# Performance work log

Measured on AMD Instinct MI355X. Metric: run time of the kernel, lower is better.

Reference implementation:

```python
import jax, jax.numpy as jnp
import numpy as np
import math

DMODEL, DK, H, DFF = 1024, 64, 16, 4096
B, T = 2, 2048
EPS = 1e-5


def setup_inputs() -> dict:
    key = jax.random.key(0)
    ks = jax.random.split(key, 12)
    s = 0.02
    x = jax.random.normal(ks[0], (B, T, DMODEL), dtype=jnp.float32)
    # causal mask, broadcastable [1,1,T,T]; 0 -> masked (like masked_fill(mask==0, -inf))
    attention_mask = jnp.tril(jnp.ones((T, T), dtype=jnp.int32))[None, None]
    Wq = jax.random.normal(ks[1], (DMODEL, DK * H), dtype=jnp.float32) * s
    bq = jnp.zeros((DK * H,), jnp.float32)
    Wk = jax.random.normal(ks[2], (DMODEL, DK * H), dtype=jnp.float32) * s
    bk = jnp.zeros((DK * H,), jnp.float32)
    Wv = jax.random.normal(ks[3], (DMODEL, DMODEL), dtype=jnp.float32) * s
    bv = jnp.zeros((DMODEL,), jnp.float32)
    W1 = jax.random.normal(ks[4], (DMODEL, DFF), dtype=jnp.float32) * s
    b1 = jnp.zeros((DFF,), jnp.float32)
    W2 = jax.random.normal(ks[5], (DFF, DMODEL), dtype=jnp.float32) * s
    b2 = jnp.zeros((DMODEL,), jnp.float32)
    g1 = jnp.ones((DMODEL,), jnp.float32)
    be1 = jnp.zeros((DMODEL,), jnp.float32)
    g2 = jnp.ones((DMODEL,), jnp.float32)
    be2 = jnp.zeros((DMODEL,), jnp.float32)
    return dict(x=x, attention_mask=attention_mask, Wq=Wq, bq=bq, Wk=Wk, bk=bk,
                Wv=Wv, bv=bv, W1=W1, b1=b1, W2=W2, b2=b2,
                g1=g1, be1=be1, g2=g2, be2=be2)


def _layernorm(x, g, b):
    mu = jnp.mean(x, axis=-1, keepdims=True)
    var = jnp.mean(jnp.square(x - mu), axis=-1, keepdims=True)
    return (x - mu) * jax.lax.rsqrt(var + EPS) * g + b


def _split_heads(t, h):  # [B,T,h*d] -> [B,h,T,d]
    Bn, Tn, D = t.shape
    return t.reshape(Bn, Tn, h, D // h).transpose(0, 2, 1, 3)


def reference(x, attention_mask, Wq, bq, Wk, bk, Wv, bv, W1, b1, W2, b2, g1, be1, g2, be2):
    # multi-head self-attention (hand-rolled, matching torch module)
    q = _split_heads(x @ Wq + bq, H)                    # [B,h,T,dk]
    k = _split_heads(x @ Wk + bk, H)                    # [B,h,T,dk]
    v = _split_heads(x @ Wv + bv, H)                    # [B,h,T,dv]
    scores = jnp.einsum('bhqd,bhkd->bhqk', q, k) / math.sqrt(DK)
    scores = jnp.where(attention_mask == 0, -jnp.inf, scores)
    probs = jax.nn.softmax(scores, axis=-1)
    attn = jnp.einsum('bhqk,bhkd->bhqd', probs, v)      # [B,h,T,dv]
    attn = attn.transpose(0, 2, 1, 3).reshape(B, T, DMODEL)
    # double residual (dropout = identity in eval): x + dropout(attn) + attn
    x1 = _layernorm(x + 2.0 * attn, g1, be1)
    ff = jax.nn.relu(x1 @ W1 + b1) @ W2 + b2
    out = _layernorm(x1 + 2.0 * ff, g2, be2)
    return out
```

## Files before the change

### kernel.cpp

```cpp
#include <hip/hip_runtime.h>

#define DMODEL 1024
#define DKH 64
#define NH 16
#define DFF 4096
#define BB 2
#define TT 2048
#define ROWS (BB*TT)
#define QKVN (3*DMODEL)

typedef unsigned short ushort_t;
typedef __attribute__((ext_vector_type(8))) short s8v;
typedef __attribute__((ext_vector_type(4))) float f4v;
typedef __attribute__((ext_vector_type(4))) unsigned short us4v;

typedef const void __attribute__((address_space(1)))* GPTR;
typedef void __attribute__((address_space(3)))* SPTR;

__device__ __forceinline__ float bf2f(ushort_t u) {
  return __uint_as_float(((unsigned int)u) << 16);
}
__device__ __forceinline__ ushort_t f2bf(float f) {
  unsigned int u = __float_as_uint(f);
  u += 0x7fffu + ((u >> 16) & 1u);
  return (ushort_t)(u >> 16);
}
__device__ __forceinline__ void gload16(const void* g, void* l) {
  __builtin_amdgcn_global_load_lds((GPTR)g, (SPTR)l, 16, 0, 0);
}

__global__ __launch_bounds__(256) void cvt_f32_bf16(const float* __restrict__ in,
                                                    ushort_t* __restrict__ out, int n4) {
  int i = blockIdx.x * 256 + threadIdx.x;
  if (i >= n4) return;
  float4 v = ((const float4*)in)[i];
  us4v o;
  o.x = f2bf(v.x); o.y = f2bf(v.y); o.z = f2bf(v.z); o.w = f2bf(v.w);
  ((us4v*)out)[i] = o;
}

__global__ __launch_bounds__(256) void transpose_cvt(const float* __restrict__ in,
                                                     ushort_t* __restrict__ out, int R, int C) {
  __shared__ float tile[32][33];
  int bx = blockIdx.x * 32, by = blockIdx.y * 32;
  int tx = threadIdx.x, ty = threadIdx.y;
#pragma unroll
  for (int i = 0; i < 32; i += 8)
    tile[ty + i][tx] = in[(size_t)(by + ty + i) * C + bx + tx];
  __syncthreads();
#pragma unroll
  for (int i = 0; i < 32; i += 8)
    out[(size_t)(bx + ty + i) * R + by + tx] = f2bf(tile[tx][ty + i]);
}

__global__ void concat_bias(const float* __restrict__ a, const float* __restrict__ b,
                            const float* __restrict__ c, float* __restrict__ o) {
  int i = blockIdx.x * 256 + threadIdx.x;
  if (i < 1024) { o[i] = a[i]; o[1024 + i] = b[i]; o[2048 + i] = c[i]; }
}

__global__ __launch_bounds__(256) void vtrans(const ushort_t* __restrict__ QKV,
                                              ushort_t* __restrict__ VT) {
  __shared__ ushort_t tile[32][66];
  const int t0 = blockIdx.x * 32;
  const int bh = blockIdx.y;
  const int b = bh >> 4, h = bh & 15;
  const int tx = threadIdx.x, ty = threadIdx.y;
  const ushort_t* src = QKV + ((size_t)b * TT + t0) * QKVN + 2 * DMODEL + h * 64;
#pragma unroll
  for (int i = 0; i < 4; ++i) {
    int r = ty + i * 8;
    *(unsigned int*)&tile[r][tx * 2] = *(const unsigned int*)(src + (size_t)r * QKVN + tx * 2);
  }
  __syncthreads();
  unsigned int* dst = (unsigned int*)(VT + (size_t)bh * 64 * TT);
#pragma unroll
  for (int i = 0; i < 4; ++i) {
    int d = ty + i * 8 + (tx >> 4) * 32;
    int p = tx & 15;
    unsigned int lo = tile[2 * p][d], hi = tile[2 * p + 1][d];
    dst[(size_t)d * (TT / 2) + (t0 >> 1) + p] = lo | (hi << 16);
  }
}

template<int MODE>
__global__ __launch_bounds__(512, 2) void gemm256(const ushort_t* __restrict__ A,
                                                  const ushort_t* __restrict__ BT,
                                                  const float* __restrict__ bias,
                                                  ushort_t* __restrict__ C,
                                                  int M, int N, int Kstride, int Kloop,
                                                  int nbx, int tiles_per_k) {
  __shared__ __align__(16) ushort_t Abuf[2][2][128 * 64];
  __shared__ __align__(16) ushort_t Bbuf[2][2][128 * 64];
  const int nwg = gridDim.x;
  const int wg = blockIdx.x;
  const int cpx = nwg >> 3;
  const int swz = (wg & 7) * cpx + (wg >> 3);
  const int ks = swz / tiles_per_k;
  const int tile = swz % tiles_per_k;
  const int bx = tile % nbx, by = tile / nbx;
  const int m0 = by * 256, n0 = bx * 256;
  const size_t kbase = (size_t)ks * Kloop;
  const int tid = threadIdx.x;
  const int w = tid >> 6, l = tid & 63, lr = l & 15, lg = l >> 4;
  const int wm = w >> 2, wn = w & 3;

  const int Ls = (tid * 16) ^ (((tid >> 5) & 1) << 5);
  const int srow = Ls >> 7;
  const int scol = (Ls & 127) >> 1;

  auto stageA = [&](int kt, int half, int buf) {
    const ushort_t* gp = A + (size_t)(m0 + half * 128 + srow) * Kstride + kbase + kt * 64 + scol;
    char* lp = (char*)&Abuf[buf][half][0] + w * 1024;
    gload16(gp, lp);
    gload16(gp + (size_t)64 * Kstride, lp + 8192);
  };
  auto stageB = [&](int kt, int half, int buf) {
    const ushort_t* gp = BT + (size_t)(n0 + half * 128 + srow) * Kstride + kbase + kt * 64 + scol;
    char* lp = (char*)&Bbuf[buf][half][0] + w * 1024;
    gload16(gp, lp);
    gload16(gp + (size_t)64 * Kstride, lp + 8192);
  };

  const int acol = lg * 16 ^ (((lr >> 2) & 1) << 5);
  auto ldA = [&](int buf, int m, int kk) -> s8v {
    return *(const s8v*)((const char*)&Abuf[buf][wm][0] + (m * 16 + lr) * 128 + kk * 64 + acol);
  };
  auto ldB = [&](int buf, int n, int kk) -> s8v {
    return *(const s8v*)((const char*)&Bbuf[buf][wn >> 1][0] +
                         ((wn & 1) * 64 + n * 16 + lr) * 128 + kk * 64 + acol);
  };

  f4v acc[8][4] = {};
  const int NT = Kloop >> 6;

  stageA(0, 0, 0); stageA(0, 1, 0); stageB(0, 0, 0); stageB(0, 1, 0);
  stageA(1, 0, 1); stageA(1, 1, 1);
  asm volatile("s_waitcnt vmcnt(4)" ::: "memory");
  __builtin_amdgcn_sched_barrier(0);
  __builtin_amdgcn_s_barrier();

  for (int t = 0; t < NT; ++t) {
    const int cb = t & 1, nb = cb ^ 1;
    s8v af[2][4], af2[2][4], bf[2][4];
#pragma unroll
    for (int m = 0; m < 4; ++m) { af[0][m] = ldA(cb, m, 0); af[1][m] = ldA(cb, m, 1); }
#pragma unroll
    for (int n = 0; n < 2; ++n) { bf[0][n] = ldB(cb, n, 0); bf[1][n] = ldB(cb, n, 1); }
    if (t + 1 < NT) stageB(t + 1, 0, nb);
    __builtin_amdgcn_s_barrier();
    asm volatile("s_waitcnt lgkmcnt(0)" ::: "memory");
    __builtin_amdgcn_s_setprio(1);
#pragma unroll
    for (int m = 0; m < 4; ++m)
#pragma unroll
      for (int n = 0; n < 2; ++n) {
        acc[m][n] = __builtin_amdgcn_mfma_f32_16x16x32_bf16(af[0][m], bf[0][n], acc[m][n], 0, 0, 0);
        acc[m][n] = __builtin_amdgcn_mfma_f32_16x16x32_bf16(af[1][m], bf[1][n], acc[m][n], 0, 0, 0);
      }
    __builtin_amdgcn_s_setprio(0);
    __builtin_amdgcn_s_barrier();
#pragma unroll
    for (int m = 0; m < 4; ++m) { af2[0][m] = ldA(cb, 4 + m, 0); af2[1][m] = ldA(cb, 4 + m, 1); }
#pragma unroll
    for (int n = 2; n < 4; ++n) { bf[0][n] = ldB(cb, n, 0); bf[1][n] = ldB(cb, n, 1); }
    if (t + 1 < NT) stageB(t + 1, 1, nb);
    __builtin_amdgcn_s_barrier();
    asm volatile("s_waitcnt lgkmcnt(0)" ::: "memory");
    __builtin_amdgcn_s_setprio(1);
#pragma unroll
    for (int m = 0; m < 4; ++m)
#pragma unroll
      for (int n = 2; n < 4; ++n) {
        acc[m][n] = __builtin_amdgcn_mfma_f32_16x16x32_bf16(af[0][m], bf[0][n], acc[m][n], 0, 0, 0);
        acc[m][n] = __builtin_amdgcn_mfma_f32_16x16x32_bf16(af[1][m], bf[1][n], acc[m][n], 0, 0, 0);
      }
    __builtin_amdgcn_s_setprio(0);
    __builtin_amdgcn_s_barrier();
    if (t + 2 < NT) { stageA(t + 2, 0, cb); stageA(t + 2, 1, cb); }
    __builtin_amdgcn_s_setprio(1);
#pragma unroll
    for (int m = 0; m < 4; ++m)
#pragma unroll
      for (int n = 0; n < 2; ++n) {
        acc[4 + m][n] = __builtin_amdgcn_mfma_f32_16x16x32_bf16(af2[0][m], bf[0][n], acc[4 + m][n], 0, 0, 0);
        acc[4 + m][n] = __builtin_amdgcn_mfma_f32_16x16x32_bf16(af2[1][m], bf[1][n], acc[4 + m][n], 0, 0, 0);
      }
#pragma unroll
    for (int m = 0; m < 4; ++m)
#pragma unroll
      for (int n = 2; n < 4; ++n) {
        acc[4 + m][n] = __builtin_amdgcn_mfma_f32_16x16x32_bf16(af2[0][m], bf[0][n], acc[4 + m][n], 0, 0, 0);
        acc[4 + m][n] = __builtin_amdgcn_mfma_f32_16x16x32_bf16(af2[1][m], bf[1][n], acc[4 + m][n], 0, 0, 0);
      }
    __builtin_amdgcn_s_setprio(0);
    if (t + 2 < NT) {
      asm volatile("s_waitcnt vmcnt(4)" ::: "memory");
    } else if (t + 1 < NT) {
      asm volatile("s_waitcnt vmcnt(0)" ::: "memory");
    }
    __builtin_amdgcn_sched_barrier(0);
    __builtin_amdgcn_s_barrier();
  }

  ushort_t* Cp = (MODE == 2) ? (C + (size_t)ks * M * N) : C;
#pragma unroll
  for (int n = 0; n < 4; ++n) {
    int col = n0 + wn * 64 + n * 16 + lr;
    float bv = (MODE == 2) ? 0.f : bias[col];
#pragma unroll
    for (int m = 0; m < 8; ++m) {
      int row = m0 + wm * 128 + m * 16 + lg * 4;
#pragma unroll
      for (int j = 0; j < 4; ++j) {
        float v = acc[m][n][j] + bv;
        if (MODE == 1) v = fmaxf(v, 0.f);
        Cp[(size_t)(row + j) * N + col] = f2bf(v);
      }
    }
  }
}

__global__ __launch_bounds__(256) void attn_kernel(const ushort_t* __restrict__ QKV,
                                                   const ushort_t* __restrict__ VT,
                                                   ushort_t* __restrict__ O) {
  const int bh = blockIdx.x;
  const int qt = 31 - (int)blockIdx.y;
  const int b = bh >> 4, h = bh & 15;
  const int nkt = qt + 1;
  const int tid = threadIdx.x;
  const int w = tid >> 6, l = tid & 63;
  const int lr = l & 15, lg = l >> 4;

  __shared__ __align__(16) ushort_t Ksh[2][64 * 64];
  __shared__ __align__(16) ushort_t Vsh[64 * 64];
  __shared__ __align__(16) ushort_t Psh[4][16 * 72];

  const size_t RS = QKVN;
  const ushort_t* Qb = QKV + (size_t)b * TT * RS + h * 64;
  const ushort_t* Kb = Qb + DMODEL;
  const ushort_t* Vb = VT + (size_t)bh * 64 * TT;

  s8v qf[2];
  {
    const ushort_t* qr = Qb + (size_t)(qt * 64 + w * 16 + lr) * RS + lg * 8;
    qf[0] = *(const s8v*)qr;
    qf[1] = *(const s8v*)(qr + 32);
  }
  f4v acc[4] = {};
  float lrow = 0.f;

  const int sr8 = l >> 3, sc = l & 7;

  auto stageK = [&](int kt, int buf) {
#pragma unroll
    for (int s = 0; s < 2; ++s) {
      int r = s * 32 + w * 8 + sr8;
      gload16(Kb + (size_t)(kt * 64 + r) * RS + ((sc ^ (r & 7)) << 3),
              (char*)&Ksh[buf][0] + (s * 32 + w * 8) * 128 + l * 16);
    }
  };
  auto stageV = [&](int kt) {
#pragma unroll
    for (int s = 0; s < 2; ++s) {
      int r = s * 32 + w * 8 + sr8;
      gload16(Vb + (size_t)r * TT + kt * 64 + ((sc ^ (r & 7)) << 3),
              (char*)&Vsh[0] + (s * 32 + w * 8) * 128 + l * 16);
    }
  };

  stageK(0, 0);
  for (int kt = 0; kt < nkt; ++kt) {
    const int cb = kt & 1;
    const bool last = (kt + 1 >= nkt);
    stageV(kt);
    if (!last) {
      stageK(kt + 1, cb ^ 1);
      asm volatile("s_waitcnt vmcnt(4)" ::: "memory");
    } else {
      asm volatile("s_waitcnt vmcnt(2)" ::: "memory");
    }
    __builtin_amdgcn_sched_barrier(0);
    __builtin_amdgcn_s_barrier();

    float ps = 0.f;
#pragma unroll
    for (int c = 0; c < 4; ++c) {
      f4v a = {};
      __builtin_amdgcn_s_setprio(1);
#pragma unroll
      for (int kk = 0; kk < 2; ++kk) {
        int rr = c * 16 + lr;
        int byte_ = (rr * 128 + kk * 64 + lg * 16) ^ ((rr & 7) << 4);
        s8v kf = *(const s8v*)((const char*)&Ksh[cb][0] + byte_);
        a = __builtin_amdgcn_mfma_f32_16x16x32_bf16(kf, qf[kk], a, 0, 0, 0);
      }
      __builtin_amdgcn_s_setprio(0);
      float e[4];
#pragma unroll
      for (int j = 0; j < 4; ++j) {
        e[j] = __expf(a[j] * 0.125f);
        if (last && (c * 16 + lg * 4 + j > w * 16 + lr)) e[j] = 0.f;
        ps += e[j];
      }
      unsigned int pk0 = (unsigned int)f2bf(e[0]) | ((unsigned int)f2bf(e[1]) << 16);
      unsigned int pk1 = (unsigned int)f2bf(e[2]) | ((unsigned int)f2bf(e[3]) << 16);
      *(uint2*)((char*)&Psh[w][0] + lr * 144 + (c * 16 + lg * 4) * 2) = make_uint2(pk0, pk1);
    }
    s8v pa[2];
    pa[0] = *(const s8v*)((const char*)&Psh[w][0] + lr * 144 + lg * 16);
    pa[1] = *(const s8v*)((const char*)&Psh[w][0] + lr * 144 + 64 + lg * 16);

    if (!last) {
      asm volatile("s_waitcnt vmcnt(2)" ::: "memory");
    } else {
      asm volatile("s_waitcnt vmcnt(0)" ::: "memory");
    }
    __builtin_amdgcn_sched_barrier(0);
    __builtin_amdgcn_s_barrier();

    __builtin_amdgcn_s_setprio(1);
#pragma unroll
    for (int ks = 0; ks < 2; ++ks)
#pragma unroll
      for (int d = 0; d < 4; ++d) {
        int row = d * 16 + lr;
        int byte_ = (row * 128 + ks * 64 + lg * 16) ^ ((row & 7) << 4);
        s8v vf = *(const s8v*)((const char*)&Vsh[0] + byte_);
        acc[d] = __builtin_amdgcn_mfma_f32_16x16x32_bf16(pa[ks], vf, acc[d], 0, 0, 0);
      }
    __builtin_amdgcn_s_setprio(0);
    ps += __shfl_xor(ps, 16);
    ps += __shfl_xor(ps, 32);
    lrow += ps;
    __builtin_amdgcn_s_barrier();
  }

  float inv = 1.f / lrow;
  ushort_t* orow = O + ((size_t)b * TT + qt * 64 + w * 16) * DMODEL + h * 64;
#pragma unroll
  for (int j = 0; j < 4; ++j) {
    float invj = __shfl(inv, lg * 4 + j);
#pragma unroll
    for (int d = 0; d < 4; ++d)
      orow[(size_t)(lg * 4 + j) * DMODEL + d * 16 + lr] = f2bf(acc[d][j] * invj);
  }
}

__global__ __launch_bounds__(256) void ln_kernel(const float* __restrict__ aptr,
                                                 const ushort_t* __restrict__ bptr,
                                                 const float* __restrict__ g,
                                                 const float* __restrict__ be,
                                                 ushort_t* __restrict__ yptr) {
  const int row = blockIdx.x;
  const int t = threadIdx.x;
  const int w = t >> 6, l = t & 63;
  const size_t base = (size_t)row * DMODEL + t * 4;
  float v[4];
  us4v bb = *(const us4v*)(bptr + base);
  float4 xa = *(const float4*)(aptr + base);
  v[0] = xa.x + 2.f * bf2f(bb.x);
  v[1] = xa.y + 2.f * bf2f(bb.y);
  v[2] = xa.z + 2.f * bf2f(bb.z);
  v[3] = xa.w + 2.f * bf2f(bb.w);
  float s = v[0] + v[1] + v[2] + v[3];
  float s2 = v[0] * v[0] + v[1] * v[1] + v[2] * v[2] + v[3] * v[3];
#pragma unroll
  for (int off = 1; off <= 32; off <<= 1) {
    s += __shfl_xor(s, off);
    s2 += __shfl_xor(s2, off);
  }
  __shared__ float red[2][4];
  if (l == 0) { red[0][w] = s; red[1][w] = s2; }
  __syncthreads();
  s = red[0][0] + red[0][1] + red[0][2] + red[0][3];
  s2 = red[1][0] + red[1][1] + red[1][2] + red[1][3];
  const float mu = s * (1.f / 1024.f);
  const float var = s2 * (1.f / 1024.f) - mu * mu;
  const float rstd = rsqrtf(var + 1e-5f);
  float4 g4 = *(const float4*)(g + t * 4);
  float4 be4 = *(const float4*)(be + t * 4);
  us4v o;
  o.x = f2bf((v[0] - mu) * rstd * g4.x + be4.x);
  o.y = f2bf((v[1] - mu) * rstd * g4.y + be4.y);
  o.z = f2bf((v[2] - mu) * rstd * g4.z + be4.z);
  o.w = f2bf((v[3] - mu) * rstd * g4.w + be4.w);
  *(us4v*)(yptr + base) = o;
}

__global__ __launch_bounds__(256) void ln2_kernel(const ushort_t* __restrict__ x1,
                                                  const ushort_t* __restrict__ part,
                                                  const float* __restrict__ b2,
                                                  const float* __restrict__ g,
                                                  const float* __restrict__ be,
                                                  float* __restrict__ y) {
  const int row = blockIdx.x;
  const int t = threadIdx.x;
  const int w = t >> 6, l = t & 63;
  const size_t base = (size_t)row * DMODEL + t * 4;
  us4v xa = *(const us4v*)(x1 + base);
  float f[4] = {0.f, 0.f, 0.f, 0.f};
#pragma unroll
  for (int ks = 0; ks < 4; ++ks) {
    us4v p = *(const us4v*)(part + (size_t)ks * ROWS * DMODEL + base);
    f[0] += bf2f(p.x); f[1] += bf2f(p.y); f[2] += bf2f(p.z); f[3] += bf2f(p.w);
  }
  float4 b2v = *(const float4*)(b2 + t * 4);
  float v[4];
  v[0] = bf2f(xa.x) + 2.f * (f[0] + b2v.x);
  v[1] = bf2f(xa.y) + 2.f * (f[1] + b2v.y);
  v[2] = bf2f(xa.z) + 2.f * (f[2] + b2v.z);
  v[3] = bf2f(xa.w) + 2.f * (f[3] + b2v.w);
  float s = v[0] + v[1] + v[2] + v[3];
  float s2 = v[0] * v[0] + v[1] * v[1] + v[2] * v[2] + v[3] * v[3];
#pragma unroll
  for (int off = 1; off <= 32; off <<= 1) {
    s += __shfl_xor(s, off);
    s2 += __shfl_xor(s2, off);
  }
  __shared__ float red[2][4];
  if (l == 0) { red[0][w] = s; red[1][w] = s2; }
  __syncthreads();
  s = red[0][0] + red[0][1] + red[0][2] + red[0][3];
  s2 = red[1][0] + red[1][1] + red[1][2] + red[1][3];
  const float mu = s * (1.f / 1024.f);
  const float var = s2 * (1.f / 1024.f) - mu * mu;
  const float rstd = rsqrtf(var + 1e-5f);
  float4 g4 = *(const float4*)(g + t * 4);
  float4 be4 = *(const float4*)(be + t * 4);
  float4 o;
  o.x = (v[0] - mu) * rstd * g4.x + be4.x;
  o.y = (v[1] - mu) * rstd * g4.y + be4.y;
  o.z = (v[2] - mu) * rstd * g4.z + be4.z;
  o.w = (v[3] - mu) * rstd * g4.w + be4.w;
  *(float4*)(y + base) = o;
}

extern "C" void kernel_launch(void* const* d_in, const int* in_sizes, int n_in,
                              void* d_out, int out_size, void* d_ws, size_t ws_size,
                              hipStream_t stream) {
  const float* x   = (const float*)d_in[0];
  const float* Wq  = (const float*)d_in[2];
  const float* bq  = (const float*)d_in[3];
  const float* Wk  = (const float*)d_in[4];
  const float* bk  = (const float*)d_in[5];
  const float* Wv  = (const float*)d_in[6];
  const float* bv  = (const float*)d_in[7];
  const float* W1  = (const float*)d_in[8];
  const float* b1  = (const float*)d_in[9];
  const float* W2  = (const float*)d_in[10];
  const float* b2  = (const float*)d_in[11];
  const float* g1  = (const float*)d_in[12];
  const float* be1 = (const float*)d_in[13];
  const float* g2  = (const float*)d_in[14];
  const float* be2 = (const float*)d_in[15];
  float* out = (float*)d_out;

  char* ws = (char*)d_ws;
  size_t off = 0;
  auto alloc = [&](size_t bytes) {
    char* p = ws + off;
    off += (bytes + 255) & ~(size_t)255;
    return p;
  };
  ushort_t* xb    = (ushort_t*)alloc((size_t)ROWS * DMODEL * 2);
  ushort_t* WqkvT = (ushort_t*)alloc((size_t)QKVN * DMODEL * 2);
  ushort_t* W1T   = (ushort_t*)alloc((size_t)DFF * DMODEL * 2);
  ushort_t* W2T   = (ushort_t*)alloc((size_t)DMODEL * DFF * 2);
  ushort_t* QKV   = (ushort_t*)alloc((size_t)ROWS * QKVN * 2);
  ushort_t* VTb   = (ushort_t*)alloc((size_t)BB * NH * 64 * TT * 2);
  ushort_t* attnb = (ushort_t*)alloc((size_t)ROWS * DMODEL * 2);
  ushort_t* x1b   = (ushort_t*)alloc((size_t)ROWS * DMODEL * 2);
  ushort_t* H1b   = (ushort_t*)alloc((size_t)ROWS * DFF * 2);
  float* qkvb     = (float*)alloc(QKVN * 4);
  ushort_t* part  = QKV;
  (void)ws_size; (void)in_sizes; (void)n_in; (void)out_size;

  dim3 b256(256);
  dim3 tb(32, 8);
  cvt_f32_bf16<<<ROWS * DMODEL / 4 / 256, b256, 0, stream>>>(x, xb, ROWS * DMODEL / 4);
  transpose_cvt<<<dim3(32, 32), tb, 0, stream>>>(Wq, WqkvT, DMODEL, DMODEL);
  transpose_cvt<<<dim3(32, 32), tb, 0, stream>>>(Wk, WqkvT + DMODEL * DMODEL, DMODEL, DMODEL);
  transpose_cvt<<<dim3(32, 32), tb, 0, stream>>>(Wv, WqkvT + 2 * DMODEL * DMODEL, DMODEL, DMODEL);
  transpose_cvt<<<dim3(DFF / 32, DMODEL / 32), tb, 0, stream>>>(W1, W1T, DMODEL, DFF);
  transpose_cvt<<<dim3(DMODEL / 32, DFF / 32), tb, 0, stream>>>(W2, W2T, DFF, DMODEL);
  concat_bias<<<4, b256, 0, stream>>>(bq, bk, bv, qkvb);

  gemm256<0><<<dim3(192), dim3(512), 0, stream>>>(xb, WqkvT, qkvb, QKV,
                                                  ROWS, QKVN, DMODEL, DMODEL,
                                                  QKVN / 256, 192);
  vtrans<<<dim3(TT / 32, BB * NH), tb, 0, stream>>>(QKV, VTb);
  attn_kernel<<<dim3(BB * NH, 32), b256, 0, stream>>>(QKV, VTb, attnb);
  ln_kernel<<<ROWS, b256, 0, stream>>>(x, attnb, g1, be1, x1b);
  gemm256<1><<<dim3(256), dim3(512), 0, stream>>>(x1b, W1T, b1, H1b,
                                                  ROWS, DFF, DMODEL, DMODEL,
                                                  DFF / 256, 256);
  gemm256<2><<<dim3(256), dim3(512), 0, stream>>>(H1b, W2T, b2, part,
                                                  ROWS, DMODEL, DFF, DFF / 4,
                                                  DMODEL / 256, 64);
  ln2_kernel<<<ROWS, b256, 0, stream>>>(x1b, part, b2, g2, be2, out);
}
```

Before: 222.9 us.

## Restructure GEMM main loop, switch LDS swizzle, use hardware bf16 pack

```diff
diff --git a/kernel.cpp b/kernel.cpp
--- a/kernel.cpp
+++ b/kernel.cpp
@@ -105,9 +105,8 @@
   const int w = tid >> 6, l = tid & 63, lr = l & 15, lg = l >> 4;
   const int wm = w >> 2, wn = w & 3;
 
-  const int Ls = (tid * 16) ^ (((tid >> 5) & 1) << 5);
-  const int srow = Ls >> 7;
-  const int scol = (Ls & 127) >> 1;
+  const int srow = tid >> 3;
+  const int scol = (((tid & 7) ^ ((tid >> 3) & 7)) << 3);
 
   auto stageA = [&](int kt, int half, int buf) {
     const ushort_t* gp = A + (size_t)(m0 + half * 128 + srow) * Kstride + kbase + kt * 64 + scol;
@@ -122,13 +121,14 @@
     gload16(gp + (size_t)64 * Kstride, lp + 8192);
   };
 
-  const int acol = lg * 16 ^ (((lr >> 2) & 1) << 5);
+  const int rsw = (lr & 7) << 4;
   auto ldA = [&](int buf, int m, int kk) -> s8v {
-    return *(const s8v*)((const char*)&Abuf[buf][wm][0] + (m * 16 + lr) * 128 + kk * 64 + acol);
+    return *(const s8v*)((const char*)&Abuf[buf][wm][0] +
+                         (m * 16 + lr) * 128 + ((kk * 64 + lg * 16) ^ rsw));
   };
   auto ldB = [&](int buf, int n, int kk) -> s8v {
     return *(const s8v*)((const char*)&Bbuf[buf][wn >> 1][0] +
-                         ((wn & 1) * 64 + n * 16 + lr) * 128 + kk * 64 + acol);
+                         ((wn & 1) * 64 + n * 16 + lr) * 128 + ((kk * 64 + lg * 16) ^ rsw));
   };
 
   f4v acc[8][4] = {};
@@ -142,58 +142,34 @@
 
   for (int t = 0; t < NT; ++t) {
     const int cb = t & 1, nb = cb ^ 1;
-    s8v af[2][4], af2[2][4], bf[2][4];
+    if (t + 1 < NT) { stageB(t + 1, 0, nb); stageB(t + 1, 1, nb); }
+    s8v af[2][4], af2[2][4], bfr[2][4];
 #pragma unroll
     for (int m = 0; m < 4; ++m) { af[0][m] = ldA(cb, m, 0); af[1][m] = ldA(cb, m, 1); }
 #pragma unroll
-    for (int n = 0; n < 2; ++n) { bf[0][n] = ldB(cb, n, 0); bf[1][n] = ldB(cb, n, 1); }
-    if (t + 1 < NT) stageB(t + 1, 0, nb);
-    __builtin_amdgcn_s_barrier();
-    asm volatile("s_waitcnt lgkmcnt(0)" ::: "memory");
+    for (int n = 0; n < 4; ++n) { bfr[0][n] = ldB(cb, n, 0); bfr[1][n] = ldB(cb, n, 1); }
     __builtin_amdgcn_s_setprio(1);
 #pragma unroll
     for (int m = 0; m < 4; ++m)
 #pragma unroll
-      for (int n = 0; n < 2; ++n) {
-        acc[m][n] = __builtin_amdgcn_mfma_f32_16x16x32_bf16(af[0][m], bf[0][n], acc[m][n], 0, 0, 0);
-        acc[m][n] = __builtin_amdgcn_mfma_f32_16x16x32_bf16(af[1][m], bf[1][n], acc[m][n], 0, 0, 0);
+      for (int n = 0; n < 4; ++n) {
+        acc[m][n] = __builtin_amdgcn_mfma_f32_16x16x32_bf16(af[0][m], bfr[0][n], acc[m][n], 0, 0, 0);
+        acc[m][n] = __builtin_amdgcn_mfma_f32_16x16x32_bf16(af[1][m], bfr[1][n], acc[m][n], 0, 0, 0);
       }
     __builtin_amdgcn_s_setprio(0);
-    __builtin_amdgcn_s_barrier();
 #pragma unroll
     for (int m = 0; m < 4; ++m) { af2[0][m] = ldA(cb, 4 + m, 0); af2[1][m] = ldA(cb, 4 + m, 1); }
-#pragma unroll
-    for (int n = 2; n < 4; ++n) { bf[0][n] = ldB(cb, n, 0); bf[1][n] = ldB(cb, n, 1); }
-    if (t + 1 < NT) stageB(t + 1, 1, nb);
-    __builtin_amdgcn_s_barrier();
-    asm volatile("s_waitcnt lgkmcnt(0)" ::: "memory");
     __builtin_amdgcn_s_setprio(1);
 #pragma unroll
     for (int m = 0; m < 4; ++m)
 #pragma unroll
-      for (int n = 2; n < 4; ++n) {
-        acc[m][n] = __builtin_amdgcn_mfma_f32_16x16x32_bf16(af[0][m], bf[0][n], acc[m][n], 0, 0, 0);
-        acc[m][n] = __builtin_amdgcn_mfma_f32_16x16x32_bf16(af[1][m], bf[1][n], acc[m][n], 0, 0, 0);
+      for (int n = 0; n < 4; ++n) {
+        acc[4 + m][n] = __builtin_amdgcn_mfma_f32_16x16x32_bf16(af2[0][m], bfr[0][n], acc[4 + m][n], 0, 0, 0);
+        acc[4 + m][n] = __builtin_amdgcn_mfma_f32_16x16x32_bf16(af2[1][m], bfr[1][n], acc[4 + m][n], 0, 0, 0);
       }
     __builtin_amdgcn_s_setprio(0);
     __builtin_amdgcn_s_barrier();
     if (t + 2 < NT) { stageA(t + 2, 0, cb); stageA(t + 2, 1, cb); }
-    __builtin_amdgcn_s_setprio(1);
-#pragma unroll
-    for (int m = 0; m < 4; ++m)
-#pragma unroll
-      for (int n = 0; n < 2; ++n) {
-        acc[4 + m][n] = __builtin_amdgcn_mfma_f32_16x16x32_bf16(af2[0][m], bf[0][n], acc[4 + m][n], 0, 0, 0);
-        acc[4 + m][n] = __builtin_amdgcn_mfma_f32_16x16x32_bf16(af2[1][m], bf[1][n], acc[4 + m][n], 0, 0, 0);
-      }
-#pragma unroll
-    for (int m = 0; m < 4; ++m)
-#pragma unroll
-      for (int n = 2; n < 4; ++n) {
-        acc[4 + m][n] = __builtin_amdgcn_mfma_f32_16x16x32_bf16(af2[0][m], bf[0][n], acc[4 + m][n], 0, 0, 0);
-        acc[4 + m][n] = __builtin_amdgcn_mfma_f32_16x16x32_bf16(af2[1][m], bf[1][n], acc[4 + m][n], 0, 0, 0);
-      }
-    __builtin_amdgcn_s_setprio(0);
     if (t + 2 < NT) {
       asm volatile("s_waitcnt vmcnt(4)" ::: "memory");
     } else if (t + 1 < NT) {
@@ -303,8 +279,9 @@
         if (last && (c * 16 + lg * 4 + j > w * 16 + lr)) e[j] = 0.f;
         ps += e[j];
       }
-      unsigned int pk0 = (unsigned int)f2bf(e[0]) | ((unsigned int)f2bf(e[1]) << 16);
-      unsigned int pk1 = (unsigned int)f2bf(e[2]) | ((unsigned int)f2bf(e[3]) << 16);
+      unsigned int pk0, pk1;
+      asm("v_cvt_pk_bf16_f32 %0, %1, %2" : "=v"(pk0) : "v"(e[0]), "v"(e[1]));
+      asm("v_cvt_pk_bf16_f32 %0, %1, %2" : "=v"(pk1) : "v"(e[2]), "v"(e[3]));
       *(uint2*)((char*)&Psh[w][0] + lr * 144 + (c * 16 + lg * 4) * 2) = make_uint2(pk0, pk1);
     }
     s8v pa[2];
```

After: 223.6 us. About the same (+0.3%).
